# Kernel optimization log

Hardware: AMD Instinct MI355X
Metric: run time of the kernel (lower is better)

The kernel has to match this reference:

```python
import jax, jax.numpy as jnp
import numpy as np

B, C, H, W = 1, 128, 48, 48
HC = 32                     # head_channel
NH = C // HC                # num heads = 4
K = 16                      # n_clusters
N = H * W                   # 2304
SCALE = HC ** 0.5
EPS = 1e-6


def setup_inputs() -> dict:
    key = jax.random.key(0)
    ks = jax.random.split(key, 20)
    s = 0.05  # weight init scale ~ xavier-ish for C=128
    def g(i, shape, sc=s):
        return jax.random.normal(ks[i], shape, dtype=jnp.float32) * sc
    return {
        'q_img': g(0, (B, C, H, W), 1.0),
        'k_img_map': g(1, (B, C, H, W), 1.0),
        'v_img_map': g(2, (B, C, H, W), 1.0),
        'pixel_coefficients': jax.random.uniform(ks[3], (B, N, N), dtype=jnp.float32),
        'labels': jax.random.randint(ks[4], (B, H, W), 0, K),
        # projections (stored as [in, out]; y = x @ w + b)
        'wq': g(5, (C, C)), 'bq': jnp.zeros((C,), jnp.float32),
        'wk': g(6, (C, C)), 'bk': jnp.zeros((C,), jnp.float32),
        'wv': g(7, (C, C)), 'bv': jnp.zeros((C,), jnp.float32),
        # mlp_1: Linear(C,2C) -> LeakyReLU(0.01) -> Linear(2C,C) (dropout=0 -> identity)
        'w1a': g(8, (C, 2 * C)), 'b1a': jnp.zeros((2 * C,), jnp.float32),
        'w1b': g(9, (2 * C, C)), 'b1b': jnp.zeros((C,), jnp.float32),
        # mlp_2
        'w2a': g(10, (C, 2 * C)), 'b2a': jnp.zeros((2 * C,), jnp.float32),
        'w2b': g(11, (2 * C, C)), 'b2b': jnp.zeros((C,), jnp.float32),
    }


def _mlp(x, wa, ba, wb, bb):
    h = x @ wa + ba
    h = jax.nn.leaky_relu(h, negative_slope=0.01)
    return h @ wb + bb


def reference(q_img, k_img_map, v_img_map, pixel_coefficients,
              wq, bq, wk, bk, wv, bv,
              w1a, b1a, w1b, b1b, w2a, b2a, w2b, b2b,
              labels):
    # projections on channel-last pixels
    q = q_img.transpose(0, 2, 3, 1).reshape(B, N, C) @ wq + bq
    k = k_img_map.transpose(0, 2, 3, 1).reshape(B, N, C) @ wk + bk
    v = v_img_map.transpose(0, 2, 3, 1).reshape(B, N, C) @ wv + bv

    labels_flat = labels.reshape(B, N)
    onehot = jax.nn.one_hot(labels_flat, K, dtype=q.dtype)        # [B,N,K]
    num_k = jnp.einsum('bnk,bnc->bkc', onehot, k)                 # [B,K,C]
    den_k = onehot.sum(axis=1)[:, :, None] + EPS                  # [B,K,1]
    centers_k = num_k / den_k

    qm = q.reshape(B, N, NH, HC).transpose(0, 2, 1, 3)            # [B,h,N,d]
    km = k.reshape(B, N, NH, HC).transpose(0, 2, 1, 3)
    vm = v.reshape(B, N, NH, HC).transpose(0, 2, 1, 3)
    kcm = centers_k.reshape(B, K, NH, HC).transpose(0, 2, 1, 3)   # [B,h,K,d]

    attn_intra = jnp.einsum('bhid,bhjd->bhij', qm, km)            # [B,h,N,N]
    attn_centers = jnp.einsum('bhid,bhkd->bhik', qm, kcm)         # [B,h,N,K]

    # gather center score per key's cluster: attn_centers[b,h,i,labels[b,j]]
    idx = jnp.broadcast_to(labels_flat[:, None, None, :], (B, NH, N, N))
    attn_inter = jnp.take_along_axis(attn_centers, idx, axis=3)   # [B,h,N,N]
    attn_inter = attn_inter * pixel_coefficients[:, None, :, :]

    same = labels_flat[:, None, :, None] == labels_flat[:, None, None, :]  # [B,1,N,N]
    scores = jnp.where(same, attn_intra, attn_inter) / SCALE
    attn_w = jax.nn.softmax(scores, axis=-1)

    out = jnp.einsum('bhij,bhjd->bhid', attn_w, vm)
    out = out.transpose(0, 2, 1, 3).reshape(B, N, C)              # [B,N,C]

    v_spatial = v.reshape(B, H, W, C).transpose(0, 3, 1, 2)       # [B,C,H,W]
    rs1 = v_spatial + _mlp(out, w1a, b1a, w1b, b1b).transpose(0, 2, 1).reshape(B, C, H, W)
    rs1_flat = rs1.transpose(0, 2, 3, 1).reshape(B, N, C)
    rs2 = rs1 + _mlp(rs1_flat, w2a, b2a, w2b, b2b).transpose(0, 2, 1).reshape(B, C, H, W)
    return rs2
```

## Files before the change

kernel.cpp:

```cpp
#include <hip/hip_runtime.h>
#include <hip/hip_bf16.h>
#include <math.h>

#define NPIX 2304
#define CCH  128
#define NH   4
#define HC   32
#define NCL  16
#define NBLK 72
#define KSPLIT 8
#define KEYS 288
#define NSTEP 9
#define QSCALE 0.25503489f

typedef __attribute__((ext_vector_type(8))) short short8;
typedef __attribute__((ext_vector_type(4))) float f32x4;

#if __has_builtin(__builtin_amdgcn_exp2f)
#define EXP2(x) __builtin_amdgcn_exp2f(x)
#else
#define EXP2(x) __expf((x) * 0.6931471805599453f)
#endif

static __device__ __forceinline__ short f2bf(float x) {
    __hip_bfloat16 b = __float2bfloat16(x);
    return *reinterpret_cast<short*>(&b);
}

#define PPT 16
__global__ void __launch_bounds__(256) proj_kernel(
        const float* __restrict__ xq, const float* __restrict__ xk,
        const float* __restrict__ xv,
        const float* __restrict__ wq, const float* __restrict__ bq,
        const float* __restrict__ wk, const float* __restrict__ bk,
        const float* __restrict__ wv, const float* __restrict__ bv,
        short* __restrict__ qbf,
        float* __restrict__ kbuf, short* __restrict__ kbf,
        float* __restrict__ vbuf, short* __restrict__ vbfT) {
    __shared__ float xs[CCH * PPT];
    const int n0 = blockIdx.x * PPT;
    const int t  = threadIdx.x;
    const int c  = t & 127;
    const int ph = t >> 7;
    const int which = blockIdx.y;
    const float* x = (which == 0) ? xq : (which == 1) ? xk : xv;
    const float* w = (which == 0) ? wq : (which == 1) ? wk : wv;
    const float* b = (which == 0) ? bq : (which == 1) ? bk : bv;

#pragma unroll
    for (int it = 0; it < 8; ++it) {
        const int flat = it * 256 + t;
        const int cc = flat >> 4;
        const int p  = flat & 15;
        xs[flat] = x[cc * NPIX + n0 + p];
    }
    __syncthreads();

    float acc[8];
    const float bb = b[c];
#pragma unroll
    for (int p = 0; p < 8; ++p) acc[p] = bb;

#pragma unroll 4
    for (int in = 0; in < CCH; ++in) {
        const float wv_ = w[in * CCH + c];
        const float4 xa = *(const float4*)(xs + in * PPT + ph * 8);
        const float4 xb = *(const float4*)(xs + in * PPT + ph * 8 + 4);
        acc[0] = fmaf(xa.x, wv_, acc[0]); acc[1] = fmaf(xa.y, wv_, acc[1]);
        acc[2] = fmaf(xa.z, wv_, acc[2]); acc[3] = fmaf(xa.w, wv_, acc[3]);
        acc[4] = fmaf(xb.x, wv_, acc[4]); acc[5] = fmaf(xb.y, wv_, acc[5]);
        acc[6] = fmaf(xb.z, wv_, acc[6]); acc[7] = fmaf(xb.w, wv_, acc[7]);
    }

    const int nb = n0 + ph * 8;
    if (which == 0) {
#pragma unroll
        for (int p = 0; p < 8; ++p)
            qbf[(size_t)(nb + p) * CCH + c] = f2bf(acc[p] * QSCALE);
    } else if (which == 1) {
#pragma unroll
        for (int p = 0; p < 8; ++p) {
            kbuf[(size_t)(nb + p) * CCH + c] = acc[p];
            kbf [(size_t)(nb + p) * CCH + c] = f2bf(acc[p]);
        }
    } else {
#pragma unroll
        for (int p = 0; p < 8; ++p) vbuf[(size_t)(nb + p) * CCH + c] = acc[p];
        short8 s0;
#pragma unroll
        for (int p = 0; p < 8; ++p) s0[p] = f2bf(acc[p]);
        *(short8*)(vbfT + (size_t)c * NPIX + nb) = s0;
    }
}

__global__ void centersA_kernel(const float* __restrict__ kbuf, const int* __restrict__ labels,
                                float* __restrict__ cpart, float* __restrict__ denpart) {
    __shared__ float ls[2 * NCL * CCH];
    __shared__ int   lab_s[32];
    __shared__ float dps[2 * NCL];
    const int b = blockIdx.x;
    const int t = threadIdx.x;
    const int g = t >> 7, c = t & 127;
    if (t < 32) lab_s[t] = labels[b * 32 + t];
    for (int u = t; u < 2 * NCL * CCH; u += 256) ls[u] = 0.f;
    __syncthreads();

    const int n0 = b * 32 + g * 16;
    for (int p = 0; p < 16; ++p) {
        const int lab = lab_s[g * 16 + p];
        ls[(g * NCL + lab) * CCH + c] += kbuf[(size_t)(n0 + p) * CCH + c];
    }
    if (t < 2 * NCL) {
        const int g2 = t >> 4, cl = t & 15;
        int cnt = 0;
        for (int p = 0; p < 16; ++p) cnt += (lab_s[g2 * 16 + p] == cl) ? 1 : 0;
        dps[t] = (float)cnt;
    }
    __syncthreads();
    for (int u = t; u < NCL * CCH; u += 256)
        cpart[(size_t)b * NCL * CCH + u] = ls[u] + ls[NCL * CCH + u];
    if (t < NCL) denpart[b * NCL + t] = dps[t] + dps[NCL + t];
}

__global__ void centersB_kernel(const float* __restrict__ cpart, const float* __restrict__ denpart,
                                short* __restrict__ cbf) {
    const int idx = blockIdx.x * 256 + threadIdx.x;
    const int kk  = idx >> 7;
    float den = 0.f;
    for (int b = 0; b < NBLK; ++b) den += denpart[b * NCL + kk];
    float s = 0.f;
    for (int b = 0; b < NBLK; ++b) s += cpart[(size_t)b * NCL * CCH + idx];
    cbf[idx] = f2bf(s / (den + 1e-6f));
}

__global__ void __launch_bounds__(256, 4) attn_part_kernel(
        const short* __restrict__ qbf,  const short* __restrict__ kbf,
        const short* __restrict__ vbfT, const short* __restrict__ cbf,
        const int* __restrict__ labels, const float* __restrict__ pc,
        float* __restrict__ part_o, float* __restrict__ part_l) {
    __shared__ __align__(16) short Pl[NH][16 * 40];
    __shared__ __align__(16) float aclT[NH][16][16];
    __shared__ int   labl[KEYS];
    const int qt   = blockIdx.x;
    const int ks   = blockIdx.y;
    const int tid  = threadIdx.x;
    const int w    = tid >> 6;
    const int lane = tid & 63;
    const int quad = lane >> 4;
    const int lq   = lane & 15;
    const int i0   = qt * 16;
    const int j0   = ks * KEYS;

    for (int u = tid; u < KEYS / 4; u += 256)
        *(int4*)(labl + u * 4) = *(const int4*)(labels + j0 + u * 4);

    const short8 aq = *(const short8*)(qbf + (size_t)(i0 + lq) * CCH + w * HC + quad * 8);

    {
        const short8 bc = *(const short8*)(cbf + (size_t)lq * CCH + w * HC + quad * 8);
        f32x4 z = {0.f, 0.f, 0.f, 0.f};
        f32x4 acd = __builtin_amdgcn_mfma_f32_16x16x32_bf16(aq, bc, z, 0, 0, 0);
        *(f32x4*)(&aclT[w][lq][quad * 4]) = acd;
    }
    int labi[4];
#pragma unroll
    for (int r = 0; r < 4; ++r) labi[r] = labels[i0 + quad * 4 + r];

    __syncthreads();

    const short* kp  = kbf  + (size_t)(j0 + lq) * CCH + w * HC + quad * 8;
    const short* vp  = vbfT + (size_t)(w * HC + lq) * NPIX + j0 + quad * 8;
    const float* pcp = pc   + (size_t)(i0 + quad * 4) * NPIX + j0 + lq;

    short8 k0A, k1A, v0A, v1A, k0B, k1B, v0B, v1B;
    float pcA[8], pcB[8];
    f32x4 accO0 = {0.f, 0.f, 0.f, 0.f};
    f32x4 accO1 = {0.f, 0.f, 0.f, 0.f};
    float lp[4] = {0.f, 0.f, 0.f, 0.f};

#define ISSUE(K0_, K1_, V0_, V1_, s) do {                                         \
        K0_ = *(const short8*)(kp + (size_t)(s) * 32 * CCH);                      \
        K1_ = *(const short8*)(kp + (size_t)((s) * 32 + 16) * CCH);               \
        V0_ = *(const short8*)(vp + (s) * 32);                                    \
        V1_ = *(const short8*)(vp + (size_t)16 * NPIX + (s) * 32);                \
    } while (0)

#define ISSUE_PC(dst, s) do {                                                     \
        _Pragma("unroll")                                                         \
        for (int r_ = 0; r_ < 4; ++r_) {                                          \
            dst[r_ * 2 + 0] = pcp[(size_t)r_ * NPIX + (s) * 32];                  \
            dst[r_ * 2 + 1] = pcp[(size_t)r_ * NPIX + (s) * 32 + 16];             \
        }                                                                         \
    } while (0)

#define COMPUTE(s, K0_, K1_, V0_, V1_, PCUSE) do {                                \
        _Pragma("unroll")                                                         \
        for (int kh = 0; kh < 2; ++kh) {                                          \
            const short8 bk = (kh == 0) ? K0_ : K1_;                              \
            f32x4 z = {0.f, 0.f, 0.f, 0.f};                                       \
            const f32x4 sv = __builtin_amdgcn_mfma_f32_16x16x32_bf16(aq, bk, z, 0, 0, 0);\
            const int slab = labl[(s) * 32 + kh * 16 + lq];                       \
            const f32x4 av4 = *(const f32x4*)(&aclT[w][slab][quad * 4]);          \
            _Pragma("unroll")                                                     \
            for (int r = 0; r < 4; ++r) {                                         \
                const float sc_ = (slab == labi[r]) ? sv[r] : av4[r] * PCUSE[r * 2 + kh];\
                const float p   = EXP2(sc_);                                      \
                lp[r] += p;                                                       \
                Pl[w][(quad * 4 + r) * 40 + kh * 16 + lq] = f2bf(p);              \
            }                                                                     \
        }                                                                         \
        const short8 ap = *(const short8*)(&Pl[w][lq * 40 + quad * 8]);           \
        accO0 = __builtin_amdgcn_mfma_f32_16x16x32_bf16(ap, V0_, accO0, 0, 0, 0); \
        accO1 = __builtin_amdgcn_mfma_f32_16x16x32_bf16(ap, V1_, accO1, 0, 0, 0); \
    } while (0)

    ISSUE(k0A, k1A, v0A, v1A, 0);
    ISSUE_PC(pcA, 0);

    for (int sb = 0; sb < NSTEP; sb += 2) {
        if (sb + 1 < NSTEP) { ISSUE(k0B, k1B, v0B, v1B, sb + 1); ISSUE_PC(pcB, sb + 1); }
        COMPUTE(sb, k0A, k1A, v0A, v1A, pcA);
        if (sb + 1 < NSTEP) {
            if (sb + 2 < NSTEP) { ISSUE(k0A, k1A, v0A, v1A, sb + 2); ISSUE_PC(pcA, sb + 2); }
            COMPUTE(sb + 1, k0B, k1B, v0B, v1B, pcB);
        }
    }
#undef ISSUE
#undef ISSUE_PC
#undef COMPUTE

#pragma unroll
    for (int r = 0; r < 4; ++r) {
        float v = lp[r];
        v += __shfl_xor(v, 1, 64);
        v += __shfl_xor(v, 2, 64);
        v += __shfl_xor(v, 4, 64);
        v += __shfl_xor(v, 8, 64);
        lp[r] = v;
    }
    if (lq == 0) {
#pragma unroll
        for (int r = 0; r < 4; ++r)
            part_l[((size_t)ks * NPIX + i0 + quad * 4 + r) * NH + w] = lp[r];
    }
#pragma unroll
    for (int r = 0; r < 4; ++r) {
        float* po = part_o + ((size_t)ks * NPIX + i0 + quad * 4 + r) * CCH + w * HC;
        po[lq]      = accO0[r];
        po[16 + lq] = accO1[r];
    }
}

__global__ void __launch_bounds__(256) mlp_h_kernel(
        const float* __restrict__ part_o, const float* __restrict__ part_l,
        const float* __restrict__ rs1,
        const float* __restrict__ wa, const float* __restrict__ ba,
        float* __restrict__ hout, int mode) {
    __shared__ float xs[16 * CCH];
    const int n0 = blockIdx.x * 16;
    const int t  = threadIdx.x;

    if (mode == 0) {
        for (int u = t; u < 512; u += 256) {
            const int p = u >> 5, c4 = (u & 31) * 4;
            const int hh = c4 >> 5;
            float ls = 0.f;
#pragma unroll
            for (int ks = 0; ks < KSPLIT; ++ks)
                ls += part_l[((size_t)ks * NPIX + n0 + p) * NH + hh];
            float sx = 0.f, sy = 0.f, sz = 0.f, sw = 0.f;
#pragma unroll
            for (int ks = 0; ks < KSPLIT; ++ks) {
                const float4 v = *(const float4*)(part_o + ((size_t)ks * NPIX + n0 + p) * CCH + c4);
                sx += v.x; sy += v.y; sz += v.z; sw += v.w;
            }
            const float inv = 1.f / ls;
            xs[p * CCH + c4 + 0] = sx * inv;
            xs[p * CCH + c4 + 1] = sy * inv;
            xs[p * CCH + c4 + 2] = sz * inv;
            xs[p * CCH + c4 + 3] = sw * inv;
        }
    } else {
        for (int u = t; u < 512; u += 256) {
            const int p = u >> 5, c4 = (u & 31) * 4;
            *(float4*)(xs + p * CCH + c4) = *(const float4*)(rs1 + (size_t)(n0 + p) * CCH + c4);
        }
    }
    __syncthreads();

    const int hh = blockIdx.y * 64 + (t & 63);
    const int pg = t >> 6;
    float acc[4];
    const float bb = ba[hh];
#pragma unroll
    for (int p = 0; p < 4; ++p) acc[p] = bb;

    for (int it = 0; it < CCH / 8; ++it) {
        float wr[8];
#pragma unroll
        for (int k = 0; k < 8; ++k) wr[k] = wa[(it * 8 + k) * 2 * CCH + hh];
#pragma unroll
        for (int p = 0; p < 4; ++p) {
            const float4 xa = *(const float4*)(xs + (pg * 4 + p) * CCH + it * 8);
            const float4 xb = *(const float4*)(xs + (pg * 4 + p) * CCH + it * 8 + 4);
            acc[p] = fmaf(xa.x, wr[0], acc[p]); acc[p] = fmaf(xa.y, wr[1], acc[p]);
            acc[p] = fmaf(xa.z, wr[2], acc[p]); acc[p] = fmaf(xa.w, wr[3], acc[p]);
            acc[p] = fmaf(xb.x, wr[4], acc[p]); acc[p] = fmaf(xb.y, wr[5], acc[p]);
            acc[p] = fmaf(xb.z, wr[6], acc[p]); acc[p] = fmaf(xb.w, wr[7], acc[p]);
        }
    }
#pragma unroll
    for (int p = 0; p < 4; ++p) {
        const float v = acc[p];
        hout[(size_t)(n0 + pg * 4 + p) * 2 * CCH + hh] = (v > 0.f) ? v : 0.01f * v;
    }
}

__global__ void __launch_bounds__(256) mlp_o_kernel(
        const float* __restrict__ hin, const float* __restrict__ res,
        const float* __restrict__ wb, const float* __restrict__ bbp,
        float* __restrict__ outp, int mode) {
    __shared__ float hs[8 * 2 * CCH];
    const int n0 = blockIdx.x * 8;
    const int t  = threadIdx.x;

    for (int u = t; u < 512; u += 256) {
        const int p = u >> 6, c4 = (u & 63) * 4;
        *(float4*)(hs + p * 2 * CCH + c4) = *(const float4*)(hin + (size_t)(n0 + p) * 2 * CCH + c4);
    }
    __syncthreads();

    const int c  = blockIdx.y * 64 + (t & 63);
    const int pg = t >> 6;
    const float bb = bbp[c];
    float a0 = bb, a1 = bb;

    for (int it = 0; it < 2 * CCH / 8; ++it) {
        float wr[8];
#pragma unroll
        for (int k = 0; k < 8; ++k) wr[k] = wb[(it * 8 + k) * CCH + c];
        const float4 ha = *(const float4*)(hs + (pg * 2 + 0) * 2 * CCH + it * 8);
        const float4 hb = *(const float4*)(hs + (pg * 2 + 0) * 2 * CCH + it * 8 + 4);
        a0 = fmaf(ha.x, wr[0], a0); a0 = fmaf(ha.y, wr[1], a0);
        a0 = fmaf(ha.z, wr[2], a0); a0 = fmaf(ha.w, wr[3], a0);
        a0 = fmaf(hb.x, wr[4], a0); a0 = fmaf(hb.y, wr[5], a0);
        a0 = fmaf(hb.z, wr[6], a0); a0 = fmaf(hb.w, wr[7], a0);
        const float4 hc = *(const float4*)(hs + (pg * 2 + 1) * 2 * CCH + it * 8);
        const float4 hd = *(const float4*)(hs + (pg * 2 + 1) * 2 * CCH + it * 8 + 4);
        a1 = fmaf(hc.x, wr[0], a1); a1 = fmaf(hc.y, wr[1], a1);
        a1 = fmaf(hc.z, wr[2], a1); a1 = fmaf(hc.w, wr[3], a1);
        a1 = fmaf(hd.x, wr[4], a1); a1 = fmaf(hd.y, wr[5], a1);
        a1 = fmaf(hd.z, wr[6], a1); a1 = fmaf(hd.w, wr[7], a1);
    }

    const int na = n0 + pg * 2, nb = na + 1;
    if (mode == 0) {
        outp[(size_t)na * CCH + c] = res[(size_t)na * CCH + c] + a0;
        outp[(size_t)nb * CCH + c] = res[(size_t)nb * CCH + c] + a1;
    } else {
        outp[(size_t)c * NPIX + na] = res[(size_t)na * CCH + c] + a0;
        outp[(size_t)c * NPIX + nb] = res[(size_t)nb * CCH + c] + a1;
    }
}

extern "C" void kernel_launch(void* const* d_in, const int* in_sizes, int n_in,
                              void* d_out, int out_size, void* d_ws, size_t ws_size,
                              hipStream_t stream) {
    const float* q_img = (const float*)d_in[0];
    const float* k_img = (const float*)d_in[1];
    const float* v_img = (const float*)d_in[2];
    const float* pc    = (const float*)d_in[3];
    const int*   labels= (const int*)  d_in[4];
    const float* wq = (const float*)d_in[5];
    const float* bq = (const float*)d_in[6];
    const float* wk = (const float*)d_in[7];
    const float* bk = (const float*)d_in[8];
    const float* wv = (const float*)d_in[9];
    const float* bv = (const float*)d_in[10];
    const float* w1a = (const float*)d_in[11];
    const float* b1a = (const float*)d_in[12];
    const float* w1b = (const float*)d_in[13];
    const float* b1b = (const float*)d_in[14];
    const float* w2a = (const float*)d_in[15];
    const float* b2a = (const float*)d_in[16];
    const float* w2b = (const float*)d_in[17];
    const float* b2b = (const float*)d_in[18];

    float* fw = (float*)d_ws;
    float* kbuf    = fw;
    float* vbuf    = kbuf + (size_t)NPIX * CCH;
    float* cpart   = vbuf + (size_t)NPIX * CCH;
    float* denpart = cpart + (size_t)NBLK * NCL * CCH;
    float* part_o  = denpart + NBLK * NCL;
    float* part_l  = part_o + (size_t)KSPLIT * NPIX * CCH;
    float* h1      = part_l + (size_t)KSPLIT * NPIX * NH;
    float* rs1     = h1 + (size_t)NPIX * 2 * CCH;
    float* h2      = rs1 + (size_t)NPIX * CCH;
    short* sw      = (short*)(h2 + (size_t)NPIX * 2 * CCH);
    short* qbf     = sw;
    short* kbf     = qbf + (size_t)NPIX * CCH;
    short* vbfT    = kbf + (size_t)NPIX * CCH;
    short* cbf     = vbfT + (size_t)NPIX * CCH;
    float* out     = (float*)d_out;

    proj_kernel<<<dim3(NPIX / PPT, 3), 256, 0, stream>>>(q_img, k_img, v_img,
                                                         wq, bq, wk, bk, wv, bv,
                                                         qbf, kbuf, kbf, vbuf, vbfT);
    centersA_kernel<<<NBLK, 256, 0, stream>>>(kbuf, labels, cpart, denpart);
    centersB_kernel<<<NCL * CCH / 256, 256, 0, stream>>>(cpart, denpart, cbf);
    attn_part_kernel<<<dim3(NPIX / 16, KSPLIT), 256, 0, stream>>>(qbf, kbf, vbfT, cbf,
                                                                  labels, pc, part_o, part_l);
    mlp_h_kernel<<<dim3(NPIX / 16, 4), 256, 0, stream>>>(part_o, part_l, nullptr,
                                                         w1a, b1a, h1, 0);
    mlp_o_kernel<<<dim3(NPIX / 8, 2), 256, 0, stream>>>(h1, vbuf, w1b, b1b, rs1, 0);
    mlp_h_kernel<<<dim3(NPIX / 16, 4), 256, 0, stream>>>(nullptr, nullptr, rs1,
                                                         w2a, b2a, h2, 1);
    mlp_o_kernel<<<dim3(NPIX / 8, 2), 256, 0, stream>>>(h2, rs1, w2b, b2b, out, 1);
}
```

Measured before the change: 184.6 us.

## Fuse all stages into one persistent kernel with global atomic barriers

Replaces the eight separate kernel launches with a single persistent kernel of 512 blocks. Stages are separated by software grid barriers built on atomic counters in workspace, which are reset by a memset before each launch. The goal is to remove per-launch overhead and the idle gaps between dependent stages. In exchange, each phase gets fewer blocks than before (attention runs 1152 work items over 512 blocks), and the design only works if all 512 blocks are co-resident, otherwise it deadlocks. It also reuses buffers (kbuf, hbuf) across stages.

```diff
diff --git a/kernel.cpp b/kernel.cpp
--- a/kernel.cpp
+++ b/kernel.cpp
@@ -12,6 +12,8 @@
 #define KEYS 288
 #define NSTEP 9
 #define QSCALE 0.25503489f
+#define PPT  16
+#define GRID 512
 
 typedef __attribute__((ext_vector_type(8))) short short8;
 typedef __attribute__((ext_vector_type(4))) float f32x4;
@@ -27,156 +29,170 @@
     return *reinterpret_cast<short*>(&b);
 }
 
-#define PPT 16
-__global__ void __launch_bounds__(256) proj_kernel(
-        const float* __restrict__ xq, const float* __restrict__ xk,
-        const float* __restrict__ xv,
-        const float* __restrict__ wq, const float* __restrict__ bq,
-        const float* __restrict__ wk, const float* __restrict__ bk,
-        const float* __restrict__ wv, const float* __restrict__ bv,
-        short* __restrict__ qbf,
-        float* __restrict__ kbuf, short* __restrict__ kbf,
-        float* __restrict__ vbuf, short* __restrict__ vbfT) {
-    __shared__ float xs[CCH * PPT];
-    const int n0 = blockIdx.x * PPT;
-    const int t  = threadIdx.x;
-    const int c  = t & 127;
-    const int ph = t >> 7;
-    const int which = blockIdx.y;
-    const float* x = (which == 0) ? xq : (which == 1) ? xk : xv;
-    const float* w = (which == 0) ? wq : (which == 1) ? wk : wv;
-    const float* b = (which == 0) ? bq : (which == 1) ? bk : bv;
-
-#pragma unroll
-    for (int it = 0; it < 8; ++it) {
-        const int flat = it * 256 + t;
-        const int cc = flat >> 4;
-        const int p  = flat & 15;
-        xs[flat] = x[cc * NPIX + n0 + p];
-    }
+struct KParams {
+    const float *xq, *xk, *xv, *pc;
+    const int   *labels;
+    const float *wq, *bq, *wk, *bk, *wv, *bv;
+    const float *w1a, *b1a, *w1b, *b1b, *w2a, *b2a, *w2b, *b2b;
+    float *kbuf, *vbuf, *cpart, *denpart, *part_o, *part_l, *rs1, *outp;
+    short *qbf, *kbf, *vbfT, *cbf;
+    int   *bar;
+};
+
+static __device__ __forceinline__ void gbar(int* cnt) {
     __syncthreads();
-
-    float acc[8];
-    const float bb = b[c];
-#pragma unroll
-    for (int p = 0; p < 8; ++p) acc[p] = bb;
-
-#pragma unroll 4
-    for (int in = 0; in < CCH; ++in) {
-        const float wv_ = w[in * CCH + c];
-        const float4 xa = *(const float4*)(xs + in * PPT + ph * 8);
-        const float4 xb = *(const float4*)(xs + in * PPT + ph * 8 + 4);
-        acc[0] = fmaf(xa.x, wv_, acc[0]); acc[1] = fmaf(xa.y, wv_, acc[1]);
-        acc[2] = fmaf(xa.z, wv_, acc[2]); acc[3] = fmaf(xa.w, wv_, acc[3]);
-        acc[4] = fmaf(xb.x, wv_, acc[4]); acc[5] = fmaf(xb.y, wv_, acc[5]);
-        acc[6] = fmaf(xb.z, wv_, acc[6]); acc[7] = fmaf(xb.w, wv_, acc[7]);
-    }
-
-    const int nb = n0 + ph * 8;
-    if (which == 0) {
-#pragma unroll
-        for (int p = 0; p < 8; ++p)
-            qbf[(size_t)(nb + p) * CCH + c] = f2bf(acc[p] * QSCALE);
-    } else if (which == 1) {
-#pragma unroll
-        for (int p = 0; p < 8; ++p) {
-            kbuf[(size_t)(nb + p) * CCH + c] = acc[p];
-            kbf [(size_t)(nb + p) * CCH + c] = f2bf(acc[p]);
-        }
-    } else {
-#pragma unroll
-        for (int p = 0; p < 8; ++p) vbuf[(size_t)(nb + p) * CCH + c] = acc[p];
-        short8 s0;
-#pragma unroll
-        for (int p = 0; p < 8; ++p) s0[p] = f2bf(acc[p]);
-        *(short8*)(vbfT + (size_t)c * NPIX + nb) = s0;
-    }
+    if (threadIdx.x == 0) {
+        __threadfence();
+        __hip_atomic_fetch_add(cnt, 1, __ATOMIC_RELAXED, __HIP_MEMORY_SCOPE_AGENT);
+        while (__hip_atomic_load(cnt, __ATOMIC_RELAXED, __HIP_MEMORY_SCOPE_AGENT) < GRID)
+            __builtin_amdgcn_s_sleep(2);
+        __threadfence();
+    }
+    __syncthreads();
 }
 
-__global__ void centersA_kernel(const float* __restrict__ kbuf, const int* __restrict__ labels,
-                                float* __restrict__ cpart, float* __restrict__ denpart) {
-    __shared__ float ls[2 * NCL * CCH];
-    __shared__ int   lab_s[32];
-    __shared__ float dps[2 * NCL];
-    const int b = blockIdx.x;
-    const int t = threadIdx.x;
-    const int g = t >> 7, c = t & 127;
-    if (t < 32) lab_s[t] = labels[b * 32 + t];
-    for (int u = t; u < 2 * NCL * CCH; u += 256) ls[u] = 0.f;
-    __syncthreads();
-
-    const int n0 = b * 32 + g * 16;
-    for (int p = 0; p < 16; ++p) {
-        const int lab = lab_s[g * 16 + p];
-        ls[(g * NCL + lab) * CCH + c] += kbuf[(size_t)(n0 + p) * CCH + c];
-    }
-    if (t < 2 * NCL) {
-        const int g2 = t >> 4, cl = t & 15;
-        int cnt = 0;
-        for (int p = 0; p < 16; ++p) cnt += (lab_s[g2 * 16 + p] == cl) ? 1 : 0;
-        dps[t] = (float)cnt;
-    }
-    __syncthreads();
-    for (int u = t; u < NCL * CCH; u += 256)
-        cpart[(size_t)b * NCL * CCH + u] = ls[u] + ls[NCL * CCH + u];
-    if (t < NCL) denpart[b * NCL + t] = dps[t] + dps[NCL + t];
-}
-
-__global__ void centersB_kernel(const float* __restrict__ cpart, const float* __restrict__ denpart,
-                                short* __restrict__ cbf) {
-    const int idx = blockIdx.x * 256 + threadIdx.x;
-    const int kk  = idx >> 7;
-    float den = 0.f;
-    for (int b = 0; b < NBLK; ++b) den += denpart[b * NCL + kk];
-    float s = 0.f;
-    for (int b = 0; b < NBLK; ++b) s += cpart[(size_t)b * NCL * CCH + idx];
-    cbf[idx] = f2bf(s / (den + 1e-6f));
-}
-
-__global__ void __launch_bounds__(256, 4) attn_part_kernel(
-        const short* __restrict__ qbf,  const short* __restrict__ kbf,
-        const short* __restrict__ vbfT, const short* __restrict__ cbf,
-        const int* __restrict__ labels, const float* __restrict__ pc,
-        float* __restrict__ part_o, float* __restrict__ part_l) {
+__global__ void __launch_bounds__(256, 2) fused_kernel(KParams P) {
+    __shared__ float xsP[CCH * PPT];
+    __shared__ float lsC[2 * NCL * CCH];
+    __shared__ int   labC[32];
+    __shared__ float dpsC[2 * NCL];
     __shared__ __align__(16) short Pl[NH][16 * 40];
     __shared__ __align__(16) float aclT[NH][16][16];
-    __shared__ int   labl[KEYS];
-    const int qt   = blockIdx.x;
-    const int ks   = blockIdx.y;
-    const int tid  = threadIdx.x;
-    const int w    = tid >> 6;
-    const int lane = tid & 63;
-    const int quad = lane >> 4;
-    const int lq   = lane & 15;
-    const int i0   = qt * 16;
-    const int j0   = ks * KEYS;
-
-    for (int u = tid; u < KEYS / 4; u += 256)
-        *(int4*)(labl + u * 4) = *(const int4*)(labels + j0 + u * 4);
-
-    const short8 aq = *(const short8*)(qbf + (size_t)(i0 + lq) * CCH + w * HC + quad * 8);
+    __shared__ __align__(16) int   labl[KEYS];
+    __shared__ float xsM[16 * CCH];
+    __shared__ float hsM[8 * 2 * CCH];
+
+    const int bid = blockIdx.x;
+    const int t   = threadIdx.x;
+
+    if (bid < 3 * 144) {
+        const int which = bid / 144;
+        const int pxblk = bid % 144;
+        const int n0    = pxblk * PPT;
+        const int c  = t & 127;
+        const int ph = t >> 7;
+        const float* x = (which == 0) ? P.xq : (which == 1) ? P.xk : P.xv;
+        const float* w = (which == 0) ? P.wq : (which == 1) ? P.wk : P.wv;
+        const float* b = (which == 0) ? P.bq : (which == 1) ? P.bk : P.bv;
+
+#pragma unroll
+        for (int it = 0; it < 8; ++it) {
+            const int flat = it * 256 + t;
+            const int cc = flat >> 4;
+            const int p  = flat & 15;
+            xsP[flat] = x[cc * NPIX + n0 + p];
+        }
+        __syncthreads();
+
+        float acc[8];
+        const float bb = b[c];
+#pragma unroll
+        for (int p = 0; p < 8; ++p) acc[p] = bb;
+
+#pragma unroll 4
+        for (int in = 0; in < CCH; ++in) {
+            const float wv_ = w[in * CCH + c];
+            const float4 xa = *(const float4*)(xsP + in * PPT + ph * 8);
+            const float4 xb = *(const float4*)(xsP + in * PPT + ph * 8 + 4);
+            acc[0] = fmaf(xa.x, wv_, acc[0]); acc[1] = fmaf(xa.y, wv_, acc[1]);
+            acc[2] = fmaf(xa.z, wv_, acc[2]); acc[3] = fmaf(xa.w, wv_, acc[3]);
+            acc[4] = fmaf(xb.x, wv_, acc[4]); acc[5] = fmaf(xb.y, wv_, acc[5]);
+            acc[6] = fmaf(xb.z, wv_, acc[6]); acc[7] = fmaf(xb.w, wv_, acc[7]);
+        }
+
+        const int nb = n0 + ph * 8;
+        if (which == 0) {
+#pragma unroll
+            for (int p = 0; p < 8; ++p)
+                P.qbf[(size_t)(nb + p) * CCH + c] = f2bf(acc[p] * QSCALE);
+        } else if (which == 1) {
+#pragma unroll
+            for (int p = 0; p < 8; ++p) {
+                P.kbuf[(size_t)(nb + p) * CCH + c] = acc[p];
+                P.kbf [(size_t)(nb + p) * CCH + c] = f2bf(acc[p]);
+            }
+        } else {
+#pragma unroll
+            for (int p = 0; p < 8; ++p) P.vbuf[(size_t)(nb + p) * CCH + c] = acc[p];
+            short8 s0;
+#pragma unroll
+            for (int p = 0; p < 8; ++p) s0[p] = f2bf(acc[p]);
+            *(short8*)(P.vbfT + (size_t)c * NPIX + nb) = s0;
+        }
+    }
+    gbar(P.bar + 0 * 16);
+
+    if (bid < NBLK) {
+        const int b = bid;
+        const int g = t >> 7, c = t & 127;
+        if (t < 32) labC[t] = P.labels[b * 32 + t];
+        for (int u = t; u < 2 * NCL * CCH; u += 256) lsC[u] = 0.f;
+        __syncthreads();
+
+        const int n0 = b * 32 + g * 16;
+        for (int p = 0; p < 16; ++p) {
+            const int lab = labC[g * 16 + p];
+            lsC[(g * NCL + lab) * CCH + c] += P.kbuf[(size_t)(n0 + p) * CCH + c];
+        }
+        if (t < 2 * NCL) {
+            const int g2 = t >> 4, cl = t & 15;
+            int cnt = 0;
+            for (int p = 0; p < 16; ++p) cnt += (labC[g2 * 16 + p] == cl) ? 1 : 0;
+            dpsC[t] = (float)cnt;
+        }
+        __syncthreads();
+        for (int u = t; u < NCL * CCH; u += 256)
+            P.cpart[(size_t)b * NCL * CCH + u] = lsC[u] + lsC[NCL * CCH + u];
+        if (t < NCL) P.denpart[b * NCL + t] = dpsC[t] + dpsC[NCL + t];
+    }
+    gbar(P.bar + 1 * 16);
+
+    if (bid < 8) {
+        const int idx = bid * 256 + t;
+        const int kk  = idx >> 7;
+        float den = 0.f;
+        for (int b = 0; b < NBLK; ++b) den += P.denpart[b * NCL + kk];
+        float s = 0.f;
+        for (int b = 0; b < NBLK; ++b) s += P.cpart[(size_t)b * NCL * CCH + idx];
+        P.cbf[idx] = f2bf(s / (den + 1e-6f));
+    }
+    gbar(P.bar + 2 * 16);
 
     {
-        const short8 bc = *(const short8*)(cbf + (size_t)lq * CCH + w * HC + quad * 8);
-        f32x4 z = {0.f, 0.f, 0.f, 0.f};
-        f32x4 acd = __builtin_amdgcn_mfma_f32_16x16x32_bf16(aq, bc, z, 0, 0, 0);
-        *(f32x4*)(&aclT[w][lq][quad * 4]) = acd;
-    }
-    int labi[4];
-#pragma unroll
-    for (int r = 0; r < 4; ++r) labi[r] = labels[i0 + quad * 4 + r];
-
-    __syncthreads();
-
-    const short* kp  = kbf  + (size_t)(j0 + lq) * CCH + w * HC + quad * 8;
-    const short* vp  = vbfT + (size_t)(w * HC + lq) * NPIX + j0 + quad * 8;
-    const float* pcp = pc   + (size_t)(i0 + quad * 4) * NPIX + j0 + lq;
-
-    short8 k0A, k1A, v0A, v1A, k0B, k1B, v0B, v1B;
-    float pcA[8], pcB[8];
-    f32x4 accO0 = {0.f, 0.f, 0.f, 0.f};
-    f32x4 accO1 = {0.f, 0.f, 0.f, 0.f};
-    float lp[4] = {0.f, 0.f, 0.f, 0.f};
+        const int w    = t >> 6;
+        const int lane = t & 63;
+        const int quad = lane >> 4;
+        const int lq   = lane & 15;
+
+        for (int vb = bid; vb < 144 * KSPLIT; vb += GRID) {
+            const int qt = vb >> 3, ks = vb & 7;
+            const int i0 = qt * 16, j0 = ks * KEYS;
+
+            __syncthreads();
+            for (int u = t; u < KEYS / 4; u += 256)
+                *(int4*)(labl + u * 4) = *(const int4*)(P.labels + j0 + u * 4);
+
+            const short8 aq = *(const short8*)(P.qbf + (size_t)(i0 + lq) * CCH + w * HC + quad * 8);
+            {
+                const short8 bc = *(const short8*)(P.cbf + (size_t)lq * CCH + w * HC + quad * 8);
+                f32x4 z = {0.f, 0.f, 0.f, 0.f};
+                f32x4 acd = __builtin_amdgcn_mfma_f32_16x16x32_bf16(aq, bc, z, 0, 0, 0);
+                *(f32x4*)(&aclT[w][lq][quad * 4]) = acd;
+            }
+            int labi[4];
+#pragma unroll
+            for (int r = 0; r < 4; ++r) labi[r] = P.labels[i0 + quad * 4 + r];
+            __syncthreads();
+
+            const short* kp  = P.kbf  + (size_t)(j0 + lq) * CCH + w * HC + quad * 8;
+            const short* vp  = P.vbfT + (size_t)(w * HC + lq) * NPIX + j0 + quad * 8;
+            const float* pcp = P.pc   + (size_t)(i0 + quad * 4) * NPIX + j0 + lq;
+
+            short8 k0A, k1A, v0A, v1A, k0B, k1B, v0B, v1B;
+            float pcA[8], pcB[8];
+            f32x4 accO0 = {0.f, 0.f, 0.f, 0.f};
+            f32x4 accO1 = {0.f, 0.f, 0.f, 0.f};
+            float lp[4] = {0.f, 0.f, 0.f, 0.f};
 
 #define ISSUE(K0_, K1_, V0_, V1_, s) do {                                         \
         K0_ = *(const short8*)(kp + (size_t)(s) * 32 * CCH);                      \
@@ -214,153 +230,153 @@
         accO1 = __builtin_amdgcn_mfma_f32_16x16x32_bf16(ap, V1_, accO1, 0, 0, 0); \
     } while (0)
 
-    ISSUE(k0A, k1A, v0A, v1A, 0);
-    ISSUE_PC(pcA, 0);
-
-    for (int sb = 0; sb < NSTEP; sb += 2) {
-        if (sb + 1 < NSTEP) { ISSUE(k0B, k1B, v0B, v1B, sb + 1); ISSUE_PC(pcB, sb + 1); }
-        COMPUTE(sb, k0A, k1A, v0A, v1A, pcA);
-        if (sb + 1 < NSTEP) {
-            if (sb + 2 < NSTEP) { ISSUE(k0A, k1A, v0A, v1A, sb + 2); ISSUE_PC(pcA, sb + 2); }
-            COMPUTE(sb + 1, k0B, k1B, v0B, v1B, pcB);
-        }
-    }
+            ISSUE(k0A, k1A, v0A, v1A, 0);
+            ISSUE_PC(pcA, 0);
+            for (int sb = 0; sb < NSTEP; sb += 2) {
+                if (sb + 1 < NSTEP) { ISSUE(k0B, k1B, v0B, v1B, sb + 1); ISSUE_PC(pcB, sb + 1); }
+                COMPUTE(sb, k0A, k1A, v0A, v1A, pcA);
+                if (sb + 1 < NSTEP) {
+                    if (sb + 2 < NSTEP) { ISSUE(k0A, k1A, v0A, v1A, sb + 2); ISSUE_PC(pcA, sb + 2); }
+                    COMPUTE(sb + 1, k0B, k1B, v0B, v1B, pcB);
+                }
+            }
 #undef ISSUE
 #undef ISSUE_PC
 #undef COMPUTE
 
 #pragma unroll
-    for (int r = 0; r < 4; ++r) {
-        float v = lp[r];
-        v += __shfl_xor(v, 1, 64);
-        v += __shfl_xor(v, 2, 64);
-        v += __shfl_xor(v, 4, 64);
-        v += __shfl_xor(v, 8, 64);
-        lp[r] = v;
-    }
-    if (lq == 0) {
-#pragma unroll
-        for (int r = 0; r < 4; ++r)
-            part_l[((size_t)ks * NPIX + i0 + quad * 4 + r) * NH + w] = lp[r];
-    }
-#pragma unroll
-    for (int r = 0; r < 4; ++r) {
-        float* po = part_o + ((size_t)ks * NPIX + i0 + quad * 4 + r) * CCH + w * HC;
-        po[lq]      = accO0[r];
-        po[16 + lq] = accO1[r];
-    }
-}
-
-__global__ void __launch_bounds__(256) mlp_h_kernel(
-        const float* __restrict__ part_o, const float* __restrict__ part_l,
-        const float* __restrict__ rs1,
-        const float* __restrict__ wa, const float* __restrict__ ba,
-        float* __restrict__ hout, int mode) {
-    __shared__ float xs[16 * CCH];
-    const int n0 = blockIdx.x * 16;
-    const int t  = threadIdx.x;
-
-    if (mode == 0) {
-        for (int u = t; u < 512; u += 256) {
-            const int p = u >> 5, c4 = (u & 31) * 4;
-            const int hh = c4 >> 5;
-            float ls = 0.f;
-#pragma unroll
-            for (int ks = 0; ks < KSPLIT; ++ks)
-                ls += part_l[((size_t)ks * NPIX + n0 + p) * NH + hh];
-            float sx = 0.f, sy = 0.f, sz = 0.f, sw = 0.f;
-#pragma unroll
-            for (int ks = 0; ks < KSPLIT; ++ks) {
-                const float4 v = *(const float4*)(part_o + ((size_t)ks * NPIX + n0 + p) * CCH + c4);
-                sx += v.x; sy += v.y; sz += v.z; sw += v.w;
-            }
-            const float inv = 1.f / ls;
-            xs[p * CCH + c4 + 0] = sx * inv;
-            xs[p * CCH + c4 + 1] = sy * inv;
-            xs[p * CCH + c4 + 2] = sz * inv;
-            xs[p * CCH + c4 + 3] = sw * inv;
-        }
-    } else {
-        for (int u = t; u < 512; u += 256) {
-            const int p = u >> 5, c4 = (u & 31) * 4;
-            *(float4*)(xs + p * CCH + c4) = *(const float4*)(rs1 + (size_t)(n0 + p) * CCH + c4);
-        }
-    }
-    __syncthreads();
-
-    const int hh = blockIdx.y * 64 + (t & 63);
-    const int pg = t >> 6;
-    float acc[4];
-    const float bb = ba[hh];
-#pragma unroll
-    for (int p = 0; p < 4; ++p) acc[p] = bb;
-
-    for (int it = 0; it < CCH / 8; ++it) {
-        float wr[8];
-#pragma unroll
-        for (int k = 0; k < 8; ++k) wr[k] = wa[(it * 8 + k) * 2 * CCH + hh];
-#pragma unroll
-        for (int p = 0; p < 4; ++p) {
-            const float4 xa = *(const float4*)(xs + (pg * 4 + p) * CCH + it * 8);
-            const float4 xb = *(const float4*)(xs + (pg * 4 + p) * CCH + it * 8 + 4);
-            acc[p] = fmaf(xa.x, wr[0], acc[p]); acc[p] = fmaf(xa.y, wr[1], acc[p]);
-            acc[p] = fmaf(xa.z, wr[2], acc[p]); acc[p] = fmaf(xa.w, wr[3], acc[p]);
-            acc[p] = fmaf(xb.x, wr[4], acc[p]); acc[p] = fmaf(xb.y, wr[5], acc[p]);
-            acc[p] = fmaf(xb.z, wr[6], acc[p]); acc[p] = fmaf(xb.w, wr[7], acc[p]);
-        }
-    }
-#pragma unroll
-    for (int p = 0; p < 4; ++p) {
-        const float v = acc[p];
-        hout[(size_t)(n0 + pg * 4 + p) * 2 * CCH + hh] = (v > 0.f) ? v : 0.01f * v;
-    }
-}
-
-__global__ void __launch_bounds__(256) mlp_o_kernel(
-        const float* __restrict__ hin, const float* __restrict__ res,
-        const float* __restrict__ wb, const float* __restrict__ bbp,
-        float* __restrict__ outp, int mode) {
-    __shared__ float hs[8 * 2 * CCH];
-    const int n0 = blockIdx.x * 8;
-    const int t  = threadIdx.x;
-
-    for (int u = t; u < 512; u += 256) {
-        const int p = u >> 6, c4 = (u & 63) * 4;
-        *(float4*)(hs + p * 2 * CCH + c4) = *(const float4*)(hin + (size_t)(n0 + p) * 2 * CCH + c4);
-    }
-    __syncthreads();
-
-    const int c  = blockIdx.y * 64 + (t & 63);
-    const int pg = t >> 6;
-    const float bb = bbp[c];
-    float a0 = bb, a1 = bb;
-
-    for (int it = 0; it < 2 * CCH / 8; ++it) {
-        float wr[8];
-#pragma unroll
-        for (int k = 0; k < 8; ++k) wr[k] = wb[(it * 8 + k) * CCH + c];
-        const float4 ha = *(const float4*)(hs + (pg * 2 + 0) * 2 * CCH + it * 8);
-        const float4 hb = *(const float4*)(hs + (pg * 2 + 0) * 2 * CCH + it * 8 + 4);
-        a0 = fmaf(ha.x, wr[0], a0); a0 = fmaf(ha.y, wr[1], a0);
-        a0 = fmaf(ha.z, wr[2], a0); a0 = fmaf(ha.w, wr[3], a0);
-        a0 = fmaf(hb.x, wr[4], a0); a0 = fmaf(hb.y, wr[5], a0);
-        a0 = fmaf(hb.z, wr[6], a0); a0 = fmaf(hb.w, wr[7], a0);
-        const float4 hc = *(const float4*)(hs + (pg * 2 + 1) * 2 * CCH + it * 8);
-        const float4 hd = *(const float4*)(hs + (pg * 2 + 1) * 2 * CCH + it * 8 + 4);
-        a1 = fmaf(hc.x, wr[0], a1); a1 = fmaf(hc.y, wr[1], a1);
-        a1 = fmaf(hc.z, wr[2], a1); a1 = fmaf(hc.w, wr[3], a1);
-        a1 = fmaf(hd.x, wr[4], a1); a1 = fmaf(hd.y, wr[5], a1);
-        a1 = fmaf(hd.z, wr[6], a1); a1 = fmaf(hd.w, wr[7], a1);
-    }
-
-    const int na = n0 + pg * 2, nb = na + 1;
-    if (mode == 0) {
-        outp[(size_t)na * CCH + c] = res[(size_t)na * CCH + c] + a0;
-        outp[(size_t)nb * CCH + c] = res[(size_t)nb * CCH + c] + a1;
-    } else {
-        outp[(size_t)c * NPIX + na] = res[(size_t)na * CCH + c] + a0;
-        outp[(size_t)c * NPIX + nb] = res[(size_t)nb * CCH + c] + a1;
-    }
+            for (int r = 0; r < 4; ++r) {
+                float v = lp[r];
+                v += __shfl_xor(v, 1, 64);
+                v += __shfl_xor(v, 2, 64);
+                v += __shfl_xor(v, 4, 64);
+                v += __shfl_xor(v, 8, 64);
+                lp[r] = v;
+            }
+            if (lq == 0) {
+#pragma unroll
+                for (int r = 0; r < 4; ++r)
+                    P.part_l[((size_t)ks * NPIX + i0 + quad * 4 + r) * NH + w] = lp[r];
+            }
+#pragma unroll
+            for (int r = 0; r < 4; ++r) {
+                float* po = P.part_o + ((size_t)ks * NPIX + i0 + quad * 4 + r) * CCH + w * HC;
+                po[lq]      = accO0[r];
+                po[16 + lq] = accO1[r];
+            }
+        }
+    }
+    gbar(P.bar + 3 * 16);
+
+#define MLP_H(MODE, XIN, WA, BA, HOUT)                                             \
+    for (int vb = bid; vb < 144 * 4; vb += GRID) {                                 \
+        const int nb_ = vb % 144, hb_ = vb / 144;                                  \
+        const int n0 = nb_ * 16;                                                   \
+        __syncthreads();                                              \
+        if (MODE == 0) {                                                           \
+            for (int u = t; u < 512; u += 256) {                                   \
+                const int p = u >> 5, c4 = (u & 31) * 4;                           \
+                const int hh2 = c4 >> 5;                                           \
+                float ls_ = 0.f;                                                   \
+                _Pragma("unroll")                                                  \
+                for (int ks = 0; ks < KSPLIT; ++ks)                                \
+                    ls_ += P.part_l[((size_t)ks * NPIX + n0 + p) * NH + hh2];      \
+                float sx = 0.f, sy = 0.f, sz = 0.f, sw2 = 0.f;                     \
+                _Pragma("unroll")                                                  \
+                for (int ks = 0; ks < KSPLIT; ++ks) {                              \
+                    const float4 v = *(const float4*)(P.part_o + ((size_t)ks * NPIX + n0 + p) * CCH + c4);\
+                    sx += v.x; sy += v.y; sz += v.z; sw2 += v.w;                   \
+                }                                                                  \
+                const float inv = 1.f / ls_;                                       \
+                xsM[p * CCH + c4 + 0] = sx * inv;                                  \
+                xsM[p * CCH + c4 + 1] = sy * inv;                                  \
+                xsM[p * CCH + c4 + 2] = sz * inv;                                  \
+                xsM[p * CCH + c4 + 3] = sw2 * inv;                                 \
+            }                                                                      \
+        } else {                                                                   \
+            for (int u = t; u < 512; u += 256) {                                   \
+                const int p = u >> 5, c4 = (u & 31) * 4;                           \
+                *(float4*)(xsM + p * CCH + c4) = *(const float4*)(XIN + (size_t)(n0 + p) * CCH + c4);\
+            }                                                                      \
+        }                                                                          \
+        __syncthreads();                                                           \
+        const int hh = hb_ * 64 + (t & 63);                                        \
+        const int pg = t >> 6;                                                     \
+        float acc[4];                                                              \
+        const float bb = BA[hh];                                                   \
+        _Pragma("unroll")                                                          \
+        for (int p = 0; p < 4; ++p) acc[p] = bb;                                   \
+        for (int it = 0; it < CCH / 8; ++it) {                                     \
+            float wr[8];                                                           \
+            _Pragma("unroll")                                                      \
+            for (int k = 0; k < 8; ++k) wr[k] = WA[(it * 8 + k) * 2 * CCH + hh];   \
+            _Pragma("unroll")                                                      \
+            for (int p = 0; p < 4; ++p) {                                          \
+                const float4 xa = *(const float4*)(xsM + (pg * 4 + p) * CCH + it * 8);\
+                const float4 xb = *(const float4*)(xsM + (pg * 4 + p) * CCH + it * 8 + 4);\
+                acc[p] = fmaf(xa.x, wr[0], acc[p]); acc[p] = fmaf(xa.y, wr[1], acc[p]);\
+                acc[p] = fmaf(xa.z, wr[2], acc[p]); acc[p] = fmaf(xa.w, wr[3], acc[p]);\
+                acc[p] = fmaf(xb.x, wr[4], acc[p]); acc[p] = fmaf(xb.y, wr[5], acc[p]);\
+                acc[p] = fmaf(xb.z, wr[6], acc[p]); acc[p] = fmaf(xb.w, wr[7], acc[p]);\
+            }                                                                      \
+        }                                                                          \
+        _Pragma("unroll")                                                          \
+        for (int p = 0; p < 4; ++p) {                                              \
+            const float v = acc[p];                                                \
+            HOUT[(size_t)(n0 + pg * 4 + p) * 2 * CCH + hh] = (v > 0.f) ? v : 0.01f * v;\
+        }                                                                          \
+    }
+
+#define MLP_O(MODE, HIN, WB, BB2, RES, OUTP)                                       \
+    for (int vb = bid; vb < 288 * 2; vb += GRID) {                                 \
+        const int nb_ = vb % 288, yb_ = vb / 288;                                  \
+        const int n0 = nb_ * 8;                                                    \
+        __syncthreads();                                              \
+        for (int u = t; u < 512; u += 256) {                                       \
+            const int p = u >> 6, c4 = (u & 63) * 4;                               \
+            *(float4*)(hsM + p * 2 * CCH + c4) = *(const float4*)(HIN + (size_t)(n0 + p) * 2 * CCH + c4);\
+        }                                                                          \
+        __syncthreads();                                                           \
+        const int c  = yb_ * 64 + (t & 63);                                        \
+        const int pg = t >> 6;                                                     \
+        const float bb = BB2[c];                                                   \
+        float a0 = bb, a1 = bb;                                                    \
+        for (int it = 0; it < 2 * CCH / 8; ++it) {                                 \
+            float wr[8];                                                           \
+            _Pragma("unroll")                                                      \
+            for (int k = 0; k < 8; ++k) wr[k] = WB[(it * 8 + k) * CCH + c];        \
+            const float4 ha = *(const float4*)(hsM + (pg * 2 + 0) * 2 * CCH + it * 8);\
+            const float4 hb = *(const float4*)(hsM + (pg * 2 + 0) * 2 * CCH + it * 8 + 4);\
+            a0 = fmaf(ha.x, wr[0], a0); a0 = fmaf(ha.y, wr[1], a0);                \
+            a0 = fmaf(ha.z, wr[2], a0); a0 = fmaf(ha.w, wr[3], a0);                \
+            a0 = fmaf(hb.x, wr[4], a0); a0 = fmaf(hb.y, wr[5], a0);                \
+            a0 = fmaf(hb.z, wr[6], a0); a0 = fmaf(hb.w, wr[7], a0);                \
+            const float4 hc = *(const float4*)(hsM + (pg * 2 + 1) * 2 * CCH + it * 8);\
+            const float4 hd = *(const float4*)(hsM + (pg * 2 + 1) * 2 * CCH + it * 8 + 4);\
+            a1 = fmaf(hc.x, wr[0], a1); a1 = fmaf(hc.y, wr[1], a1);                \
+            a1 = fmaf(hc.z, wr[2], a1); a1 = fmaf(hc.w, wr[3], a1);                \
+            a1 = fmaf(hd.x, wr[4], a1); a1 = fmaf(hd.y, wr[5], a1);                \
+            a1 = fmaf(hd.z, wr[6], a1); a1 = fmaf(hd.w, wr[7], a1);                \
+        }                                                                          \
+        const int na = n0 + pg * 2, nb2 = na + 1;                                  \
+        if (MODE == 0) {                                                           \
+            OUTP[(size_t)na * CCH + c]  = RES[(size_t)na * CCH + c] + a0;          \
+            OUTP[(size_t)nb2 * CCH + c] = RES[(size_t)nb2 * CCH + c] + a1;         \
+        } else {                                                                   \
+            OUTP[(size_t)c * NPIX + na]  = RES[(size_t)na * CCH + c] + a0;         \
+            OUTP[(size_t)c * NPIX + nb2] = RES[(size_t)nb2 * CCH + c] + a1;        \
+        }                                                                          \
+    }
+
+    MLP_H(0, P.rs1 , P.w1a, P.b1a, P.rs1 )
+    gbar(P.bar + 4 * 16);
+    MLP_O(0, P.rs1 , P.w1b, P.b1b, P.vbuf, P.kbuf )
+    gbar(P.bar + 5 * 16);
+    MLP_H(1, P.kbuf , P.w2a, P.b2a, P.rs1 )
+    gbar(P.bar + 6 * 16);
+    MLP_O(1, P.rs1 , P.w2b, P.b2b, P.kbuf , P.outp)
+#undef MLP_H
+#undef MLP_O
 }
 
 extern "C" void kernel_launch(void* const* d_in, const int* in_sizes, int n_in,
@@ -371,20 +387,6 @@
     const float* v_img = (const float*)d_in[2];
     const float* pc    = (const float*)d_in[3];
     const int*   labels= (const int*)  d_in[4];
-    const float* wq = (const float*)d_in[5];
-    const float* bq = (const float*)d_in[6];
-    const float* wk = (const float*)d_in[7];
-    const float* bk = (const float*)d_in[8];
-    const float* wv = (const float*)d_in[9];
-    const float* bv = (const float*)d_in[10];
-    const float* w1a = (const float*)d_in[11];
-    const float* b1a = (const float*)d_in[12];
-    const float* w1b = (const float*)d_in[13];
-    const float* b1b = (const float*)d_in[14];
-    const float* w2a = (const float*)d_in[15];
-    const float* b2a = (const float*)d_in[16];
-    const float* w2b = (const float*)d_in[17];
-    const float* b2b = (const float*)d_in[18];
 
     float* fw = (float*)d_ws;
     float* kbuf    = fw;
@@ -393,27 +395,27 @@
     float* denpart = cpart + (size_t)NBLK * NCL * CCH;
     float* part_o  = denpart + NBLK * NCL;
     float* part_l  = part_o + (size_t)KSPLIT * NPIX * CCH;
-    float* h1      = part_l + (size_t)KSPLIT * NPIX * NH;
-    float* rs1     = h1 + (size_t)NPIX * 2 * CCH;
-    float* h2      = rs1 + (size_t)NPIX * CCH;
-    short* sw      = (short*)(h2 + (size_t)NPIX * 2 * CCH);
+    float* hbuf    = part_l + (size_t)KSPLIT * NPIX * NH;
+    short* sw      = (short*)(hbuf + (size_t)NPIX * 2 * CCH);
     short* qbf     = sw;
     short* kbf     = qbf + (size_t)NPIX * CCH;
     short* vbfT    = kbf + (size_t)NPIX * CCH;
     short* cbf     = vbfT + (size_t)NPIX * CCH;
-    float* out     = (float*)d_out;
-
-    proj_kernel<<<dim3(NPIX / PPT, 3), 256, 0, stream>>>(q_img, k_img, v_img,
-                                                         wq, bq, wk, bk, wv, bv,
-                                                         qbf, kbuf, kbf, vbuf, vbfT);
-    centersA_kernel<<<NBLK, 256, 0, stream>>>(kbuf, labels, cpart, denpart);
-    centersB_kernel<<<NCL * CCH / 256, 256, 0, stream>>>(cpart, denpart, cbf);
-    attn_part_kernel<<<dim3(NPIX / 16, KSPLIT), 256, 0, stream>>>(qbf, kbf, vbfT, cbf,
-                                                                  labels, pc, part_o, part_l);
-    mlp_h_kernel<<<dim3(NPIX / 16, 4), 256, 0, stream>>>(part_o, part_l, nullptr,
-                                                         w1a, b1a, h1, 0);
-    mlp_o_kernel<<<dim3(NPIX / 8, 2), 256, 0, stream>>>(h1, vbuf, w1b, b1b, rs1, 0);
-    mlp_h_kernel<<<dim3(NPIX / 16, 4), 256, 0, stream>>>(nullptr, nullptr, rs1,
-                                                         w2a, b2a, h2, 1);
-    mlp_o_kernel<<<dim3(NPIX / 8, 2), 256, 0, stream>>>(h2, rs1, w2b, b2b, out, 1);
+    int*   bar     = (int*)((char*)d_ws + (size_t)32 * 1024 * 1024);
+
+    KParams P;
+    P.xq = q_img; P.xk = k_img; P.xv = v_img; P.pc = pc; P.labels = labels;
+    P.wq = (const float*)d_in[5];  P.bq = (const float*)d_in[6];
+    P.wk = (const float*)d_in[7];  P.bk = (const float*)d_in[8];
+    P.wv = (const float*)d_in[9];  P.bv = (const float*)d_in[10];
+    P.w1a = (const float*)d_in[11]; P.b1a = (const float*)d_in[12];
+    P.w1b = (const float*)d_in[13]; P.b1b = (const float*)d_in[14];
+    P.w2a = (const float*)d_in[15]; P.b2a = (const float*)d_in[16];
+    P.w2b = (const float*)d_in[17]; P.b2b = (const float*)d_in[18];
+    P.kbuf = kbuf; P.vbuf = vbuf; P.cpart = cpart; P.denpart = denpart;
+    P.part_o = part_o; P.part_l = part_l; P.rs1 = hbuf; P.outp = (float*)d_out;
+    P.qbf = qbf; P.kbf = kbf; P.vbfT = vbfT; P.cbf = cbf; P.bar = bar;
+
+    hipMemsetAsync(bar, 0, 512, stream);
+    fused_kernel<<<dim3(GRID), dim3(256), 0, stream>>>(P);
 }
```

Result: slower. 516.5 us (+179.8%).
